# Optimization experiments

Measured on AMD Instinct MI355X. Metric: run time of the kernel, lower is better.

Reference implementation:

```python
import jax, jax.numpy as jnp
import numpy as np

M = 7          # init kwarg m
TAU = 3        # init kwarg tau
C_IN = 7       # init kwarg c_in
KSIZE = M + 1  # 8
NUM_KERNELS = 74
PAD = M * TAU  # 21, left-pad only
RAND_CH = 0    # original uses torch.randint at forward time; fixed for determinism


def setup_inputs() -> dict:
    key = jax.random.key(0)
    k1, k2 = jax.random.split(key)
    x = jax.random.normal(k1, (32, 8192, C_IN), dtype=jnp.float32)
    # learned parameter: self.kernels, shape [num_kernels, kernel_size]
    kernels = jax.random.normal(k2, (NUM_KERNELS, KSIZE), dtype=jnp.float32)
    return {"x": x, "kernels": kernels}


def reference(x, kernels):
    B, S, C = x.shape
    # pad left with zeros on time axis: [B, C, S+PAD]
    xp = jnp.pad(jnp.transpose(x, (0, 2, 1)), ((0, 0), (0, 0), (PAD, 0)))
    W = (S + PAD - KSIZE) // TAU + 1  # number of unfolded windows
    idx = jnp.arange(W)[:, None] * TAU + jnp.arange(KSIZE)[None, :]  # [W, K]
    windows = xp[:, :, idx]  # [B, C, W, K]
    # The 73-iteration depthwise conv1d loop (each output length 1) is exactly a
    # dot product of each window with each kernel. torch.cat over the loop is
    # kernel-major in the channel dim -> layout [B, W, n, C] -> [B, W, n*C].
    main = jnp.einsum('bcwk,nk->bwnc', windows, kernels[:NUM_KERNELS - 1])
    main = main.reshape(B, W, (NUM_KERNELS - 1) * C)
    # final feature: one selected channel convolved with the last kernel
    final = jnp.einsum('bwk,k->bw', windows[:, RAND_CH], kernels[-1])[..., None]
    combined = jnp.concatenate([main, final], axis=2)  # [B, W, 73*C+1]
    return jnp.transpose(combined, (0, 2, 1))[:, :, :S]
```

## Files before the change

kernel.cpp:

```cpp
#include <hip/hip_runtime.h>


typedef float f32x4 __attribute__((ext_vector_type(4)));

constexpr int Bn   = 32;
constexpr int Sn   = 8192;
constexpr int Cn   = 7;
constexpr int Kn   = 8;
constexpr int PADn = 21;
constexpr int Wn   = 2736;
constexpr int OCH  = 512;
constexpr int MAXCH = 60;
constexpr int SAMP = (MAXCH - 1) * 12 + 17;
constexpr int CSTR = 728;

__global__ __launch_bounds__(256)
void conv_v9(const float* __restrict__ x, const float* __restrict__ kern,
             float* __restrict__ out) {
    __shared__ float lx[Cn * CSTR];

    const int tid = threadIdx.x;
    const int wq  = blockIdx.x;
    const int gp  = blockIdx.y;
    const int b   = blockIdx.z;

    const int cht  = 56 + ((wq < 3) ? 4 : 0);
    const int coff = 56 * wq + 4 * ((wq < 3) ? wq : 3);
    const int samp = (cht - 1) * 12 + 17;

    const int g0 = (12 * coff - PADn) * Cn;
    const float* xb = x + (size_t)b * Sn * Cn;
    for (int i = tid; i < samp * Cn; i += 256) {
        int gg = g0 + i;
        float v = (gg >= 0 && gg < Sn * Cn) ? xb[gg] : 0.0f;
        int s = i / 7;
        int c = i - 7 * s;
        lx[c * CSTR + s] = v;
    }
    __syncthreads();

    const int lane = tid & 63;
    const int r    = __builtin_amdgcn_readfirstlane(tid >> 6);
    if (lane >= cht) return;

    const int n0 = gp ? 36 : 0;
    const int n1 = gp ? 73 : 36;

    float* ob = out + (size_t)b * OCH * Wn + 4 * (coff + lane);
    const int sloc = 12 * lane;

    for (int c = 0; c < Cn; ++c) {
        const float* lr = lx + c * CSTR + sloc;
        float xw[17];
        *reinterpret_cast<f32x4*>(xw + 0)  = *reinterpret_cast<const f32x4*>(lr + 0);
        *reinterpret_cast<f32x4*>(xw + 4)  = *reinterpret_cast<const f32x4*>(lr + 4);
        *reinterpret_cast<f32x4*>(xw + 8)  = *reinterpret_cast<const f32x4*>(lr + 8);
        *reinterpret_cast<f32x4*>(xw + 12) = *reinterpret_cast<const f32x4*>(lr + 12);
        xw[16] = lr[16];

        for (int n = n0 + r; n < n1; n += 4) {
            const float* kr = kern + n * Kn;
            float a0 = 0.f, a1 = 0.f, a2 = 0.f, a3 = 0.f;
#pragma unroll
            for (int k = 0; k < 8; ++k) {
                float kv = kr[k];
                a0 = fmaf(xw[0 + k], kv, a0);
                a1 = fmaf(xw[3 + k], kv, a1);
                a2 = fmaf(xw[6 + k], kv, a2);
                a3 = fmaf(xw[9 + k], kv, a3);
            }
            f32x4 o = {a0, a1, a2, a3};
            *reinterpret_cast<f32x4*>(ob + (size_t)(n * 7 + c) * Wn) = o;
        }
        if (c == 0 && gp == 1 && r == 3) {
            const float* kr = kern + 73 * Kn;
            float a0 = 0.f, a1 = 0.f, a2 = 0.f, a3 = 0.f;
#pragma unroll
            for (int k = 0; k < 8; ++k) {
                float kv = kr[k];
                a0 = fmaf(xw[0 + k], kv, a0);
                a1 = fmaf(xw[3 + k], kv, a1);
                a2 = fmaf(xw[6 + k], kv, a2);
                a3 = fmaf(xw[9 + k], kv, a3);
            }
            f32x4 o = {a0, a1, a2, a3};
            *reinterpret_cast<f32x4*>(ob + (size_t)511 * Wn) = o;
        }
    }
}

extern "C" void kernel_launch(void* const* d_in, const int* in_sizes, int n_in,
                              void* d_out, int out_size, void* d_ws, size_t ws_size,
                              hipStream_t stream) {
    const float* x    = (const float*)d_in[0];
    const float* kern = (const float*)d_in[1];
    float* out        = (float*)d_out;

    conv_v9<<<dim3(12, 2, Bn), 256, 0, stream>>>(x, kern, out);
}
```

Baseline: 38.26 us.

## Merge kernel-group blocks and give each thread two window chunks

Removes the two-way split over kernel groups, so each block handles all 73 kernels with 8 waves of 512 threads. The time range per block grows to 84-88 chunks of four windows, and each lane covers two chunks, sharing kernel-weight loads across them. This loads each input tile into shared memory once instead of twice and cuts the grid from 768 to 256 blocks. The trade-off is fewer blocks to fill the GPU, more registers per thread, and idle lanes in the second chunk.

```diff
diff --git a/kernel.cpp b/kernel.cpp
--- a/kernel.cpp
+++ b/kernel.cpp
@@ -10,27 +10,26 @@
 constexpr int PADn = 21;
 constexpr int Wn   = 2736;
 constexpr int OCH  = 512;
-constexpr int MAXCH = 60;
-constexpr int SAMP = (MAXCH - 1) * 12 + 17;
-constexpr int CSTR = 728;
+constexpr int MAXCH = 88;
+constexpr int MAXSAMP = MAXCH * 12 + 5;
+constexpr int CSTR = 1064;
 
-__global__ __launch_bounds__(256)
-void conv_v9(const float* __restrict__ x, const float* __restrict__ kern,
-             float* __restrict__ out) {
+__global__ __launch_bounds__(512)
+void conv_v10(const float* __restrict__ x, const float* __restrict__ kern,
+              float* __restrict__ out) {
     __shared__ float lx[Cn * CSTR];
 
     const int tid = threadIdx.x;
     const int wq  = blockIdx.x;
-    const int gp  = blockIdx.y;
-    const int b   = blockIdx.z;
+    const int b   = blockIdx.y;
 
-    const int cht  = 56 + ((wq < 3) ? 4 : 0);
-    const int coff = 56 * wq + 4 * ((wq < 3) ? wq : 3);
-    const int samp = (cht - 1) * 12 + 17;
+    const int cht  = (wq < 3) ? 88 : 84;
+    const int coff = (wq < 3) ? 88 * wq : 264 + 84 * (wq - 3);
+    const int samp = cht * 12 + 5;
 
     const int g0 = (12 * coff - PADn) * Cn;
     const float* xb = x + (size_t)b * Sn * Cn;
-    for (int i = tid; i < samp * Cn; i += 256) {
+    for (int i = tid; i < samp * Cn; i += 512) {
         int gg = g0 + i;
         float v = (gg >= 0 && gg < Sn * Cn) ? xb[gg] : 0.0f;
         int s = i / 7;
@@ -41,50 +40,93 @@
 
     const int lane = tid & 63;
     const int r    = __builtin_amdgcn_readfirstlane(tid >> 6);
-    if (lane >= cht) return;
+    const int ch0  = lane;
+    const int ch1  = lane + 64;
+    const bool p1  = (ch1 < cht);
 
-    const int n0 = gp ? 36 : 0;
-    const int n1 = gp ? 73 : 36;
-
-    float* ob = out + (size_t)b * OCH * Wn + 4 * (coff + lane);
-    const int sloc = 12 * lane;
+    float* ob = out + (size_t)b * OCH * Wn + 4 * coff;
 
     for (int c = 0; c < Cn; ++c) {
-        const float* lr = lx + c * CSTR + sloc;
-        float xw[17];
-        *reinterpret_cast<f32x4*>(xw + 0)  = *reinterpret_cast<const f32x4*>(lr + 0);
-        *reinterpret_cast<f32x4*>(xw + 4)  = *reinterpret_cast<const f32x4*>(lr + 4);
-        *reinterpret_cast<f32x4*>(xw + 8)  = *reinterpret_cast<const f32x4*>(lr + 8);
-        *reinterpret_cast<f32x4*>(xw + 12) = *reinterpret_cast<const f32x4*>(lr + 12);
-        xw[16] = lr[16];
+        const float* lc = lx + c * CSTR;
+        float xw0[17], xw1[17];
+        {
+            const float* lr = lc + 12 * ch0;
+            *reinterpret_cast<f32x4*>(xw0 + 0)  = *reinterpret_cast<const f32x4*>(lr + 0);
+            *reinterpret_cast<f32x4*>(xw0 + 4)  = *reinterpret_cast<const f32x4*>(lr + 4);
+            *reinterpret_cast<f32x4*>(xw0 + 8)  = *reinterpret_cast<const f32x4*>(lr + 8);
+            *reinterpret_cast<f32x4*>(xw0 + 12) = *reinterpret_cast<const f32x4*>(lr + 12);
+            xw0[16] = lr[16];
+        }
+        if (p1) {
+            const float* lr = lc + 12 * ch1;
+            *reinterpret_cast<f32x4*>(xw1 + 0)  = *reinterpret_cast<const f32x4*>(lr + 0);
+            *reinterpret_cast<f32x4*>(xw1 + 4)  = *reinterpret_cast<const f32x4*>(lr + 4);
+            *reinterpret_cast<f32x4*>(xw1 + 8)  = *reinterpret_cast<const f32x4*>(lr + 8);
+            *reinterpret_cast<f32x4*>(xw1 + 12) = *reinterpret_cast<const f32x4*>(lr + 12);
+            xw1[16] = lr[16];
+        }
 
-        for (int n = n0 + r; n < n1; n += 4) {
+        for (int n = r; n < 73; n += 8) {
             const float* kr = kern + n * Kn;
-            float a0 = 0.f, a1 = 0.f, a2 = 0.f, a3 = 0.f;
+            float kv[8];
 #pragma unroll
-            for (int k = 0; k < 8; ++k) {
-                float kv = kr[k];
-                a0 = fmaf(xw[0 + k], kv, a0);
-                a1 = fmaf(xw[3 + k], kv, a1);
-                a2 = fmaf(xw[6 + k], kv, a2);
-                a3 = fmaf(xw[9 + k], kv, a3);
+            for (int k = 0; k < 8; ++k) kv[k] = kr[k];
+            float* orow = ob + (size_t)(n * 7 + c) * Wn;
+            {
+                float a0 = 0.f, a1 = 0.f, a2 = 0.f, a3 = 0.f;
+#pragma unroll
+                for (int k = 0; k < 8; ++k) {
+                    a0 = fmaf(xw0[0 + k], kv[k], a0);
+                    a1 = fmaf(xw0[3 + k], kv[k], a1);
+                    a2 = fmaf(xw0[6 + k], kv[k], a2);
+                    a3 = fmaf(xw0[9 + k], kv[k], a3);
+                }
+                f32x4 o = {a0, a1, a2, a3};
+                *reinterpret_cast<f32x4*>(orow + 4 * ch0) = o;
             }
-            f32x4 o = {a0, a1, a2, a3};
-            *reinterpret_cast<f32x4*>(ob + (size_t)(n * 7 + c) * Wn) = o;
+            if (p1) {
+                float a0 = 0.f, a1 = 0.f, a2 = 0.f, a3 = 0.f;
+#pragma unroll
+                for (int k = 0; k < 8; ++k) {
+                    a0 = fmaf(xw1[0 + k], kv[k], a0);
+                    a1 = fmaf(xw1[3 + k], kv[k], a1);
+                    a2 = fmaf(xw1[6 + k], kv[k], a2);
+                    a3 = fmaf(xw1[9 + k], kv[k], a3);
+                }
+                f32x4 o = {a0, a1, a2, a3};
+                *reinterpret_cast<f32x4*>(orow + 4 * ch1) = o;
+            }
         }
-        if (c == 0 && gp == 1 && r == 3) {
+        if (c == 0 && r == 7) {
             const float* kr = kern + 73 * Kn;
-            float a0 = 0.f, a1 = 0.f, a2 = 0.f, a3 = 0.f;
+            float kv[8];
 #pragma unroll
-            for (int k = 0; k < 8; ++k) {
-                float kv = kr[k];
-                a0 = fmaf(xw[0 + k], kv, a0);
-                a1 = fmaf(xw[3 + k], kv, a1);
-                a2 = fmaf(xw[6 + k], kv, a2);
-                a3 = fmaf(xw[9 + k], kv, a3);
+            for (int k = 0; k < 8; ++k) kv[k] = kr[k];
+            float* orow = ob + (size_t)511 * Wn;
+            {
+                float a0 = 0.f, a1 = 0.f, a2 = 0.f, a3 = 0.f;
+#pragma unroll
+                for (int k = 0; k < 8; ++k) {
+                    a0 = fmaf(xw0[0 + k], kv[k], a0);
+                    a1 = fmaf(xw0[3 + k], kv[k], a1);
+                    a2 = fmaf(xw0[6 + k], kv[k], a2);
+                    a3 = fmaf(xw0[9 + k], kv[k], a3);
+                }
+                f32x4 o = {a0, a1, a2, a3};
+                *reinterpret_cast<f32x4*>(orow + 4 * ch0) = o;
             }
-            f32x4 o = {a0, a1, a2, a3};
-            *reinterpret_cast<f32x4*>(ob + (size_t)511 * Wn) = o;
+            if (p1) {
+                float a0 = 0.f, a1 = 0.f, a2 = 0.f, a3 = 0.f;
+#pragma unroll
+                for (int k = 0; k < 8; ++k) {
+                    a0 = fmaf(xw1[0 + k], kv[k], a0);
+                    a1 = fmaf(xw1[3 + k], kv[k], a1);
+                    a2 = fmaf(xw1[6 + k], kv[k], a2);
+                    a3 = fmaf(xw1[9 + k], kv[k], a3);
+                }
+                f32x4 o = {a0, a1, a2, a3};
+                *reinterpret_cast<f32x4*>(orow + 4 * ch1) = o;
+            }
         }
     }
 }
@@ -96,5 +138,5 @@
     const float* kern = (const float*)d_in[1];
     float* out        = (float*)d_out;
 
-    conv_v9<<<dim3(12, 2, Bn), 256, 0, stream>>>(x, kern, out);
+    conv_v10<<<dim3(8, Bn), 512, 0, stream>>>(x, kern, out);
 }
```

Result: no change. 38.71 us (+1.2%).
